# Performance work log

Hardware: AMD Instinct MI355X
Metric: run time of the kernel (lower is better)

Reference implementation:

```python
import jax, jax.numpy as jnp
import numpy as np

H = 12       # num attention heads
D = 64       # head dim
K = 6        # heads activated: max(1, int(H * top_k_percent)), top_k_percent=0.5
EPS = 1e-12  # BERT LayerNorm eps


def setup_inputs() -> dict:
    key = jax.random.key(0)
    ks = jax.random.split(key, 8)
    hid = H * D
    sc = 0.02
    return {
        'hidden_states': jax.random.normal(ks[0], (8, 1024, hid), jnp.float32),
        'Wq': jax.random.normal(ks[1], (hid, hid), jnp.float32) * sc,
        'bq': jnp.zeros((hid,), jnp.float32),
        'Wk': jax.random.normal(ks[2], (hid, hid), jnp.float32) * sc,
        'bk': jnp.zeros((hid,), jnp.float32),
        'Wv': jax.random.normal(ks[3], (hid, hid), jnp.float32) * sc,
        'bv': jnp.zeros((hid,), jnp.float32),
        'Wr': jax.random.normal(ks[4], (hid, H), jnp.float32) * sc,
        'br': jnp.zeros((H,), jnp.float32),
        'Wo': jax.random.normal(ks[5], (hid, hid), jnp.float32) * sc,
        'bo': jnp.zeros((hid,), jnp.float32),
        'ln_g': jnp.ones((hid,), jnp.float32),
        'ln_b': jnp.zeros((hid,), jnp.float32),
    }


def reference(hidden_states, Wq, bq, Wk, bk, Wv, bv, Wr, br, Wo, bo, ln_g, ln_b):
    B, S, hid = hidden_states.shape
    # Router: mean-pooled tokens -> per-head logits -> straight-through top-k mask
    router_in = hidden_states.mean(axis=1)                      # [B, hid]
    logits = router_in @ Wr + br                                # [B, H]
    _, top_idx = jax.lax.top_k(logits, K)                       # [B, K]
    hard = jax.nn.one_hot(top_idx, H, dtype=logits.dtype).sum(axis=1)  # [B, H]
    head_mask = hard + logits - jax.lax.stop_gradient(logits)   # straight-through
    m = head_mask[:, :, None, None]                             # [B, H, 1, 1]

    def proj(W, b):
        return (hidden_states @ W + b).reshape(B, S, H, D).transpose(0, 2, 1, 3)

    q = proj(Wq, bq) * m
    k = proj(Wk, bk) * m
    v = proj(Wv, bv) * m

    scores = jnp.einsum('bhqd,bhkd->bhqk', q, k) / jnp.sqrt(jnp.float32(D))
    probs = jax.nn.softmax(scores, axis=-1)
    ctx = jnp.einsum('bhqk,bhkd->bhqd', probs, v)               # [B, H, S, D]
    ctx = ctx.transpose(0, 2, 1, 3).reshape(B, S, hid)

    # BertSelfOutput: dense -> (dropout=identity in eval) -> residual -> LayerNorm
    x = ctx @ Wo + bo + hidden_states
    mu = x.mean(axis=-1, keepdims=True)
    var = ((x - mu) ** 2).mean(axis=-1, keepdims=True)
    return ((x - mu) / jnp.sqrt(var + EPS)) * ln_g + ln_b
```

## Files before the change

### kernel.cpp

```cpp
#include <hip/hip_runtime.h>

typedef __bf16 bf16;
typedef __bf16 bf16x4_t __attribute__((ext_vector_type(4)));
typedef __bf16 bf16x8 __attribute__((ext_vector_type(8)));
typedef float  f32x4  __attribute__((ext_vector_type(4)));

__device__ __forceinline__ void async16(const void* g, void* l) {
  __builtin_amdgcn_global_load_lds(
      (__attribute__((address_space(1))) void*)(g),
      (__attribute__((address_space(3))) void*)(l), 16, 0, 0);
}

__device__ __forceinline__ f32x4 mfma16(bf16x8 a, bf16x8 b, f32x4 c) {
  return __builtin_amdgcn_mfma_f32_16x16x32_bf16(a, b, c, 0, 0, 0);
}

__global__ __launch_bounds__(256) void cvt_hs_k(const float* __restrict__ src,
                                                bf16* __restrict__ dst, int n) {
  int i = (blockIdx.x * 256 + threadIdx.x) * 4;
  if (i + 3 < n) {
    float4 v = *(const float4*)(src + i);
    dst[i]     = (bf16)v.x;
    dst[i + 1] = (bf16)v.y;
    dst[i + 2] = (bf16)v.z;
    dst[i + 3] = (bf16)v.w;
  } else {
    for (int j = 0; j < 4 && i + j < n; ++j) dst[i + j] = (bf16)src[i + j];
  }
}

__global__ __launch_bounds__(256) void transpose4_k(
    const float* __restrict__ s0, const float* __restrict__ s1,
    const float* __restrict__ s2, const float* __restrict__ s3,
    bf16* __restrict__ d0, bf16* __restrict__ d1,
    bf16* __restrict__ d2, bf16* __restrict__ d3) {
  __shared__ bf16 tile[32][33];
  int z = blockIdx.z;
  const float* in = (z == 0) ? s0 : (z == 1) ? s1 : (z == 2) ? s2 : s3;
  bf16* out       = (z == 0) ? d0 : (z == 1) ? d1 : (z == 2) ? d2 : d3;
  int c0 = blockIdx.x * 32, r0 = blockIdx.y * 32;
  int t = threadIdx.x;
#pragma unroll
  for (int i = 0; i < 4; ++i) {
    int idx = t + i * 256;
    int r = idx >> 5, c = idx & 31;
    tile[r][c] = (bf16)in[(size_t)(r0 + r) * 768 + (c0 + c)];
  }
  __syncthreads();
#pragma unroll
  for (int i = 0; i < 4; ++i) {
    int idx = t + i * 256;
    int r = idx >> 5, c = idx & 31;
    out[(size_t)(c0 + r) * 768 + (r0 + c)] = tile[c][r];
  }
}

__global__ __launch_bounds__(256) void router_partial_k(const float* __restrict__ hs,
                                                        float* __restrict__ partial) {
  int b = blockIdx.x, g = blockIdx.y, t = threadIdx.x;
  if (t >= 192) return;
  const float* p = hs + ((size_t)b * 1024 + g * 64) * 768 + t * 4;
  float4 a = {0.f, 0.f, 0.f, 0.f};
  for (int s = 0; s < 64; ++s) {
    float4 v = *(const float4*)(p + (size_t)s * 768);
    a.x += v.x; a.y += v.y; a.z += v.z; a.w += v.w;
  }
  *(float4*)(partial + ((size_t)b * 16 + g) * 768 + t * 4) = a;
}

__global__ __launch_bounds__(256) void router_final_k(const float* __restrict__ Wr,
                                                      const float* __restrict__ br,
                                                      const float* __restrict__ partial,
                                                      float* __restrict__ mask) {
  int b = blockIdx.x, t = threadIdx.x;
  __shared__ float mean_s[768];
  __shared__ float lg[12];
  for (int c = t; c < 768; c += 256) {
    float a = 0.f;
    for (int g = 0; g < 16; ++g) a += partial[((size_t)b * 16 + g) * 768 + c];
    mean_s[c] = a * (1.0f / 1024.0f);
  }
  __syncthreads();
  if (t < 12) {
    float a = br[t];
    for (int c = 0; c < 768; ++c) a += mean_s[c] * Wr[c * 12 + t];
    lg[t] = a;
  }
  __syncthreads();
  if (t == 0) {
    unsigned chosen = 0;
    for (int j = 0; j < 6; ++j) {
      int bi = -1; float bv = -1e30f;
      for (int h = 0; h < 12; ++h)
        if (!((chosen >> h) & 1) && lg[h] > bv) { bv = lg[h]; bi = h; }
      chosen |= 1u << bi;
    }
    for (int h = 0; h < 12; ++h) mask[b * 12 + h] = ((chosen >> h) & 1) ? 1.f : 0.f;
  }
}

__global__ __launch_bounds__(256, 3) void gemm_qkv_k(
    const bf16* __restrict__ X, const bf16* __restrict__ Wcat,
    const float* __restrict__ bq, const float* __restrict__ bk, const float* __restrict__ bv,
    bf16* __restrict__ Qo, bf16* __restrict__ Ko, bf16* __restrict__ Vto) {
  __shared__ __align__(16) bf16 Al[128 * 64];
  __shared__ __align__(16) bf16 Bl[128 * 64];
  int bid = blockIdx.x;
  int xcd = bid & 7, idx = bid >> 3;
  int nt = idx % 18, mt8 = idx / 18;
  int m0 = (mt8 * 8 + xcd) * 128;
  int n0 = nt * 128;
  int z = nt / 6;
  int nb0 = n0 - z * 768;
  const float* bia = (z == 0) ? bq : (z == 1) ? bk : bv;
  int t = threadIdx.x, w = t >> 6, lane = t & 63, lrow = lane & 15, quad = lane >> 4;
  int wm = (w >> 1) * 64, wn = (w & 1) * 64;

  int srow = t >> 3;
  int sch  = (t & 7) ^ (srow & 7);
  const bf16* aptr[4];
  const bf16* bptr[4];
#pragma unroll
  for (int i = 0; i < 4; ++i) {
    aptr[i] = X    + (size_t)(m0 + i * 32 + srow) * 768 + sch * 8;
    bptr[i] = Wcat + (size_t)(n0 + i * 32 + srow) * 768 + sch * 8;
  }

  int ra_base = wm + lrow, rb_base = wn + lrow;
  const bf16* baA[2];
  const bf16* baB[2];
#pragma unroll
  for (int ks = 0; ks < 2; ++ks) {
    baA[ks] = &Al[ra_base * 64 + (((ks * 4 + quad) ^ (ra_base & 7)) * 8)];
    baB[ks] = &Bl[rb_base * 64 + (((ks * 4 + quad) ^ (rb_base & 7)) * 8)];
  }

  f32x4 acc[4][4];
#pragma unroll
  for (int a = 0; a < 4; ++a)
#pragma unroll
    for (int b = 0; b < 4; ++b) acc[a][b] = (f32x4){0.f, 0.f, 0.f, 0.f};

  for (int k0 = 0; k0 < 768; k0 += 64) {
#pragma unroll
    for (int i = 0; i < 4; ++i) {
      async16(aptr[i], &Al[(i * 256 + t) * 8]);
      aptr[i] += 64;
    }
#pragma unroll
    for (int i = 0; i < 4; ++i) {
      async16(bptr[i], &Bl[(i * 256 + t) * 8]);
      bptr[i] += 64;
    }
    __syncthreads();
    bf16x8 af[2][4], bfr[2][4];
#pragma unroll
    for (int ks = 0; ks < 2; ++ks)
#pragma unroll
      for (int i = 0; i < 4; ++i) {
        af[ks][i]  = *(const bf16x8*)(baA[ks] + i * 1024);
        bfr[ks][i] = *(const bf16x8*)(baB[ks] + i * 1024);
      }
#pragma unroll
    for (int ks = 0; ks < 2; ++ks)
#pragma unroll
      for (int mt = 0; mt < 4; ++mt)
#pragma unroll
        for (int nt2 = 0; nt2 < 4; ++nt2)
          acc[mt][nt2] = mfma16(af[ks][mt], bfr[ks][nt2], acc[mt][nt2]);
    __syncthreads();
  }

  float biasv[4];
#pragma unroll
  for (int nt2 = 0; nt2 < 4; ++nt2) biasv[nt2] = bia[nb0 + wn + nt2 * 16 + lrow];

  if (z == 2) {
#pragma unroll
    for (int mt = 0; mt < 4; ++mt)
#pragma unroll
      for (int nt2 = 0; nt2 < 4; ++nt2) {
        int s_base = m0 + wm + mt * 16 + quad * 4;
        int bb = s_base >> 10, s = s_base & 1023;
        int nl = nb0 + wn + nt2 * 16 + lrow;
        int h = nl >> 6, d = nl & 63;
        bf16x4_t pk;
#pragma unroll
        for (int r = 0; r < 4; ++r) pk[r] = (bf16)(acc[mt][nt2][r] + biasv[nt2]);
        *(bf16x4_t*)&Vto[(((size_t)bb * 12 + h) * 64 + d) * 1024 + s] = pk;
      }
  } else {
    bf16* Out = (z == 0) ? Qo : Ko;
#pragma unroll
    for (int mt = 0; mt < 4; ++mt)
#pragma unroll
      for (int nt2 = 0; nt2 < 4; ++nt2)
#pragma unroll
        for (int r = 0; r < 4; ++r) {
          int m = m0 + wm + mt * 16 + quad * 4 + r;
          int nl = nb0 + wn + nt2 * 16 + lrow;
          int bb = m >> 10, s = m & 1023, h = nl >> 6, d = nl & 63;
          Out[(((size_t)bb * 12 + h) * 1024 + s) * 64 + d] =
              (bf16)(acc[mt][nt2][r] + biasv[nt2]);
        }
  }
}

__global__ __launch_bounds__(256) void attn_k(
    const bf16* __restrict__ Q, const bf16* __restrict__ K, const bf16* __restrict__ Vt,
    const float* __restrict__ mask, bf16* __restrict__ ctx) {
  int qt = blockIdx.x, bh = blockIdx.y;
  int b = bh / 12, h = bh % 12;
  int t = threadIdx.x, w = t >> 6, lane = t & 63, lrow = lane & 15, quad = lane >> 4;

  if (mask[bh] == 0.f) {
    for (int i = t; i < 4096; i += 256) {
      int r = i >> 5, c = i & 31;
      size_t e = ((size_t)(b * 1024 + qt * 128 + r)) * 768 + h * 64;
      ((unsigned*)ctx)[e / 2 + c] = 0u;
    }
    return;
  }

  __shared__ __align__(16) bf16 K_lds[128 * 64];
  __shared__ __align__(16) bf16 V_lds[64 * 128];
  __shared__ __align__(16) bf16 P_lds[4][32 * 136];

  const bf16* Qh = Q  + (size_t)bh * 65536;
  const bf16* Kh = K  + (size_t)bh * 65536;
  const bf16* Vh = Vt + (size_t)bh * 65536;

  bf16x8 qf[2][2];
#pragma unroll
  for (int mt = 0; mt < 2; ++mt)
#pragma unroll
    for (int ks = 0; ks < 2; ++ks)
      qf[mt][ks] = *(const bf16x8*)&Qh[(size_t)(qt * 128 + w * 32 + mt * 16 + lrow) * 64 + ks * 32 + quad * 8];

  f32x4 o_acc[2][4];
  float m_i[2][4], l_i[2][4];
#pragma unroll
  for (int mt = 0; mt < 2; ++mt) {
#pragma unroll
    for (int dt = 0; dt < 4; ++dt) o_acc[mt][dt] = (f32x4){0.f, 0.f, 0.f, 0.f};
#pragma unroll
    for (int r = 0; r < 4; ++r) { m_i[mt][r] = -INFINITY; l_i[mt][r] = 0.f; }
  }

  for (int kt = 0; kt < 8; ++kt) {
#pragma unroll
    for (int i = 0; i < 4; ++i) {
      int c = i * 256 + t;
      int r = c >> 3, ch = (c & 7) ^ (r & 7);
      async16(Kh + (size_t)kt * 8192 + r * 64 + ch * 8, &K_lds[c * 8]);
    }
#pragma unroll
    for (int i = 0; i < 4; ++i) {
      int c = i * 256 + t;
      int r = c >> 4, ch = (c & 15) ^ (r & 7);
      async16(Vh + (size_t)r * 1024 + kt * 128 + ch * 8, &V_lds[c * 8]);
    }
    __syncthreads();

    f32x4 s_acc[2][8];
#pragma unroll
    for (int mt = 0; mt < 2; ++mt)
#pragma unroll
      for (int nt = 0; nt < 8; ++nt) s_acc[mt][nt] = (f32x4){0.f, 0.f, 0.f, 0.f};
#pragma unroll
    for (int nt = 0; nt < 8; ++nt) {
      int rb = nt * 16 + lrow;
#pragma unroll
      for (int ks = 0; ks < 2; ++ks) {
        bf16x8 kf = *(const bf16x8*)&K_lds[rb * 64 + (((ks * 4 + quad) ^ (rb & 7)) * 8)];
        s_acc[0][nt] = mfma16(qf[0][ks], kf, s_acc[0][nt]);
        s_acc[1][nt] = mfma16(qf[1][ks], kf, s_acc[1][nt]);
      }
    }
#pragma unroll
    for (int mt = 0; mt < 2; ++mt)
#pragma unroll
      for (int nt = 0; nt < 8; ++nt) s_acc[mt][nt] = s_acc[mt][nt] * 0.125f;

#pragma unroll
    for (int mt = 0; mt < 2; ++mt) {
#pragma unroll
      for (int r = 0; r < 4; ++r) {
        float mx = s_acc[mt][0][r];
#pragma unroll
        for (int nt = 1; nt < 8; ++nt) mx = fmaxf(mx, s_acc[mt][nt][r]);
        mx = fmaxf(mx, __shfl_xor(mx, 1));
        mx = fmaxf(mx, __shfl_xor(mx, 2));
        mx = fmaxf(mx, __shfl_xor(mx, 4));
        mx = fmaxf(mx, __shfl_xor(mx, 8));
        float mold = m_i[mt][r];
        float mnew = fmaxf(mold, mx);
        float alpha = __expf(mold - mnew);
        m_i[mt][r] = mnew;
        float rs = 0.f;
#pragma unroll
        for (int nt = 0; nt < 8; ++nt) {
          float pv = __expf(s_acc[mt][nt][r] - mnew);
          rs += pv;
          P_lds[w][(mt * 16 + quad * 4 + r) * 136 + nt * 16 + lrow] = (bf16)pv;
        }
        rs += __shfl_xor(rs, 1);
        rs += __shfl_xor(rs, 2);
        rs += __shfl_xor(rs, 4);
        rs += __shfl_xor(rs, 8);
        l_i[mt][r] = l_i[mt][r] * alpha + rs;
#pragma unroll
        for (int dt = 0; dt < 4; ++dt) o_acc[mt][dt][r] *= alpha;
      }
    }
    __syncthreads();

#pragma unroll
    for (int dt = 0; dt < 4; ++dt) {
      int rv = dt * 16 + lrow;
#pragma unroll
      for (int ks = 0; ks < 4; ++ks) {
        bf16x8 vf = *(const bf16x8*)&V_lds[rv * 128 + (((ks * 4 + quad) ^ (rv & 7)) * 8)];
#pragma unroll
        for (int mt = 0; mt < 2; ++mt) {
          bf16x8 pf = *(const bf16x8*)&P_lds[w][(mt * 16 + lrow) * 136 + ks * 32 + quad * 8];
          o_acc[mt][dt] = mfma16(pf, vf, o_acc[mt][dt]);
        }
      }
    }
    __syncthreads();
  }

#pragma unroll
  for (int mt = 0; mt < 2; ++mt)
#pragma unroll
    for (int r = 0; r < 4; ++r) {
      float inv = 1.0f / l_i[mt][r];
      int s = qt * 128 + w * 32 + mt * 16 + quad * 4 + r;
#pragma unroll
      for (int dt = 0; dt < 4; ++dt) {
        int d = dt * 16 + lrow;
        ctx[((size_t)(b * 1024 + s)) * 768 + h * 64 + d] = (bf16)(o_acc[mt][dt][r] * inv);
      }
    }
}

__global__ __launch_bounds__(256, 3) void gemm_out_k(
    const bf16* __restrict__ Cx, const bf16* __restrict__ Wot,
    const float* __restrict__ bo, const float* __restrict__ res,
    float* __restrict__ xo) {
  __shared__ __align__(16) bf16 Al[128 * 64];
  __shared__ __align__(16) bf16 Bl[128 * 64];
  int bid = blockIdx.x;
  int xcd = bid & 7, idx = bid >> 3;
  int nt = idx % 6, mt8 = idx / 6;
  int m0 = (mt8 * 8 + xcd) * 128;
  int n0 = nt * 128;
  int t = threadIdx.x, w = t >> 6, lane = t & 63, lrow = lane & 15, quad = lane >> 4;
  int wm = (w >> 1) * 64, wn = (w & 1) * 64;

  int srow = t >> 3;
  int sch  = (t & 7) ^ (srow & 7);
  const bf16* aptr[4];
  const bf16* bptr[4];
#pragma unroll
  for (int i = 0; i < 4; ++i) {
    aptr[i] = Cx  + (size_t)(m0 + i * 32 + srow) * 768 + sch * 8;
    bptr[i] = Wot + (size_t)(n0 + i * 32 + srow) * 768 + sch * 8;
  }
  int ra_base = wm + lrow, rb_base = wn + lrow;
  const bf16* baA[2];
  const bf16* baB[2];
#pragma unroll
  for (int ks = 0; ks < 2; ++ks) {
    baA[ks] = &Al[ra_base * 64 + (((ks * 4 + quad) ^ (ra_base & 7)) * 8)];
    baB[ks] = &Bl[rb_base * 64 + (((ks * 4 + quad) ^ (rb_base & 7)) * 8)];
  }

  f32x4 acc[4][4];
#pragma unroll
  for (int a = 0; a < 4; ++a)
#pragma unroll
    for (int b = 0; b < 4; ++b) acc[a][b] = (f32x4){0.f, 0.f, 0.f, 0.f};

  for (int k0 = 0; k0 < 768; k0 += 64) {
#pragma unroll
    for (int i = 0; i < 4; ++i) {
      async16(aptr[i], &Al[(i * 256 + t) * 8]);
      aptr[i] += 64;
    }
#pragma unroll
    for (int i = 0; i < 4; ++i) {
      async16(bptr[i], &Bl[(i * 256 + t) * 8]);
      bptr[i] += 64;
    }
    __syncthreads();
    bf16x8 af[2][4], bfr[2][4];
#pragma unroll
    for (int ks = 0; ks < 2; ++ks)
#pragma unroll
      for (int i = 0; i < 4; ++i) {
        af[ks][i]  = *(const bf16x8*)(baA[ks] + i * 1024);
        bfr[ks][i] = *(const bf16x8*)(baB[ks] + i * 1024);
      }
#pragma unroll
    for (int ks = 0; ks < 2; ++ks)
#pragma unroll
      for (int mt = 0; mt < 4; ++mt)
#pragma unroll
        for (int nt2 = 0; nt2 < 4; ++nt2)
          acc[mt][nt2] = mfma16(af[ks][mt], bfr[ks][nt2], acc[mt][nt2]);
    __syncthreads();
  }

  float biasv[4];
#pragma unroll
  for (int nt2 = 0; nt2 < 4; ++nt2) biasv[nt2] = bo[n0 + wn + nt2 * 16 + lrow];

#pragma unroll
  for (int mt = 0; mt < 4; ++mt)
#pragma unroll
    for (int nt2 = 0; nt2 < 4; ++nt2)
#pragma unroll
      for (int r = 0; r < 4; ++r) {
        int m = m0 + wm + mt * 16 + quad * 4 + r;
        int n = n0 + wn + nt2 * 16 + lrow;
        xo[(size_t)m * 768 + n] = acc[mt][nt2][r] + biasv[nt2] + res[(size_t)m * 768 + n];
      }
}

__global__ __launch_bounds__(256) void ln_k(const float* __restrict__ x,
                                            const float* __restrict__ g,
                                            const float* __restrict__ be,
                                            float* __restrict__ out) {
  int row = blockIdx.x, t = threadIdx.x;
  const float* xr = x + (size_t)row * 768;
  float v0 = xr[t], v1 = xr[t + 256], v2 = xr[t + 512];
  float s = v0 + v1 + v2;
  float s2 = v0 * v0 + v1 * v1 + v2 * v2;
#pragma unroll
  for (int off = 32; off > 0; off >>= 1) {
    s  += __shfl_down(s, off);
    s2 += __shfl_down(s2, off);
  }
  __shared__ float red[8];
  if ((t & 63) == 0) { red[(t >> 6) * 2] = s; red[(t >> 6) * 2 + 1] = s2; }
  __syncthreads();
  if (t == 0) {
    float a = 0.f, b2 = 0.f;
    for (int i = 0; i < 4; ++i) { a += red[2 * i]; b2 += red[2 * i + 1]; }
    float mu = a * (1.0f / 768.0f);
    float var = b2 * (1.0f / 768.0f) - mu * mu;
    red[0] = mu;
    red[1] = rsqrtf(var + 1e-12f);
  }
  __syncthreads();
  float mu = red[0], rs = red[1];
  out[(size_t)row * 768 + t]       = (v0 - mu) * rs * g[t]       + be[t];
  out[(size_t)row * 768 + t + 256] = (v1 - mu) * rs * g[t + 256] + be[t + 256];
  out[(size_t)row * 768 + t + 512] = (v2 - mu) * rs * g[t + 512] + be[t + 512];
}

extern "C" void kernel_launch(void* const* d_in, const int* in_sizes, int n_in,
                              void* d_out, int out_size, void* d_ws, size_t ws_size,
                              hipStream_t stream) {
  const float* hs  = (const float*)d_in[0];
  const float* Wq  = (const float*)d_in[1];
  const float* bq  = (const float*)d_in[2];
  const float* Wk  = (const float*)d_in[3];
  const float* bk  = (const float*)d_in[4];
  const float* Wv  = (const float*)d_in[5];
  const float* bv  = (const float*)d_in[6];
  const float* Wr  = (const float*)d_in[7];
  const float* br  = (const float*)d_in[8];
  const float* Wo  = (const float*)d_in[9];
  const float* bo  = (const float*)d_in[10];
  const float* lng = (const float*)d_in[11];
  const float* lnb = (const float*)d_in[12];
  float* out = (float*)d_out;
  dim3 blk(256);

  char* p = (char*)d_ws;
  float* maskp   = (float*)p; p += 512;
  float* partial = (float*)p; p += (size_t)8 * 16 * 768 * 4;
  bf16* hsb  = (bf16*)p; p += (size_t)8192 * 768 * 2;
  bf16* Wcat = (bf16*)p; p += (size_t)2304 * 768 * 2;
  bf16* Wot  = (bf16*)p; p += (size_t)768 * 768 * 2;

  cvt_hs_k<<<dim3(6144), blk, 0, stream>>>(hs, hsb, 6291456);
  transpose4_k<<<dim3(24, 24, 4), blk, 0, stream>>>(
      Wq, Wk, Wv, Wo, Wcat, Wcat + 768 * 768, Wcat + 1536 * 768, Wot);
  router_partial_k<<<dim3(8, 16), blk, 0, stream>>>(hs, partial);
  router_final_k<<<dim3(8), blk, 0, stream>>>(Wr, br, partial, maskp);

  size_t used_common = (size_t)(p - (char*)d_ws);
  size_t need_big = used_common + 3 * (size_t)8192 * 768 * 2;

  if (ws_size >= need_big) {
    char* qk_base = p;
    bf16* Qb  = (bf16*)p; p += (size_t)8192 * 768 * 2;
    bf16* Kb  = (bf16*)p; p += (size_t)8192 * 768 * 2;
    bf16* Vtb = (bf16*)p;
    float* Xb = (float*)qk_base;
    bf16* Ctx = (bf16*)d_out;

    gemm_qkv_k<<<dim3(8 * 8 * 18), blk, 0, stream>>>(hsb, Wcat, bq, bk, bv, Qb, Kb, Vtb);
    attn_k<<<dim3(8, 96), blk, 0, stream>>>(Qb, Kb, Vtb, maskp, Ctx);
    gemm_out_k<<<dim3(8 * 8 * 6), blk, 0, stream>>>(Ctx, Wot, bo, hs, Xb);
    ln_k<<<dim3(8192), blk, 0, stream>>>(Xb, lng, lnb, out);
  } else {
    bf16* Qb  = (bf16*)p; p += (size_t)1024 * 768 * 2;
    bf16* Kb  = (bf16*)p; p += (size_t)1024 * 768 * 2;
    bf16* Vtb = (bf16*)p; p += (size_t)1024 * 768 * 2;
    bf16* Ctx = (bf16*)p; p += (size_t)1024 * 768 * 2;
    float* Xb = (float*)p; p += (size_t)1024 * 768 * 4;

    for (int b = 0; b < 8; ++b) {
      const bf16* hsb_b = hsb + (size_t)b * 1024 * 768;
      const float* hs_b = hs + (size_t)b * 1024 * 768;
      float* outb = out + (size_t)b * 1024 * 768;
      gemm_qkv_k<<<dim3(8 * 1 * 18), blk, 0, stream>>>(hsb_b, Wcat, bq, bk, bv, Qb, Kb, Vtb);
      attn_k<<<dim3(8, 12), blk, 0, stream>>>(Qb, Kb, Vtb, maskp + b * 12, Ctx);
      gemm_out_k<<<dim3(8 * 1 * 6), blk, 0, stream>>>(Ctx, Wot, bo, hs_b, Xb);
      ln_k<<<dim3(1024), blk, 0, stream>>>(Xb, lng, lnb, outb);
    }
  }
}
```

Measured before the change: 252.5 us.

## Skip masked-head GEMM tiles and keep attention probabilities in registers

The QKV projection now exits early for output tiles whose two heads are both masked off. The output projection skips K-chunks that belong to inactive heads, since their context rows are zero. The attention kernel computes S transposed, so row max and sum reductions reduce to cross-quad shuffles, and it builds the P operand for the PV MFMA through lane shuffles instead of an LDS round trip. This removes the per-warp P buffer and one barrier per key tile, at the cost of more shuffle instructions and a changed block order.

```diff
diff --git a/kernel.cpp b/kernel.cpp
--- a/kernel.cpp
+++ b/kernel.cpp
@@ -1,6 +1,7 @@
 #include <hip/hip_runtime.h>
 
 typedef __bf16 bf16;
+typedef __bf16 bf16x2_t __attribute__((ext_vector_type(2)));
 typedef __bf16 bf16x4_t __attribute__((ext_vector_type(4)));
 typedef __bf16 bf16x8 __attribute__((ext_vector_type(8)));
 typedef float  f32x4  __attribute__((ext_vector_type(4)));
@@ -102,6 +103,7 @@
 __global__ __launch_bounds__(256, 3) void gemm_qkv_k(
     const bf16* __restrict__ X, const bf16* __restrict__ Wcat,
     const float* __restrict__ bq, const float* __restrict__ bk, const float* __restrict__ bv,
+    const float* __restrict__ mask,
     bf16* __restrict__ Qo, bf16* __restrict__ Ko, bf16* __restrict__ Vto) {
   __shared__ __align__(16) bf16 Al[128 * 64];
   __shared__ __align__(16) bf16 Bl[128 * 64];
@@ -112,6 +114,9 @@
   int n0 = nt * 128;
   int z = nt / 6;
   int nb0 = n0 - z * 768;
+  int bb = m0 >> 10, hh0 = nb0 >> 6;
+  if (mask[bb * 12 + hh0] == 0.f && mask[bb * 12 + hh0 + 1] == 0.f) return;
+
   const float* bia = (z == 0) ? bq : (z == 1) ? bk : bv;
   int t = threadIdx.x, w = t >> 6, lane = t & 63, lrow = lane & 15, quad = lane >> 4;
   int wm = (w >> 1) * 64, wn = (w & 1) * 64;
@@ -181,13 +186,13 @@
 #pragma unroll
       for (int nt2 = 0; nt2 < 4; ++nt2) {
         int s_base = m0 + wm + mt * 16 + quad * 4;
-        int bb = s_base >> 10, s = s_base & 1023;
+        int bb2 = s_base >> 10, s = s_base & 1023;
         int nl = nb0 + wn + nt2 * 16 + lrow;
         int h = nl >> 6, d = nl & 63;
         bf16x4_t pk;
 #pragma unroll
         for (int r = 0; r < 4; ++r) pk[r] = (bf16)(acc[mt][nt2][r] + biasv[nt2]);
-        *(bf16x4_t*)&Vto[(((size_t)bb * 12 + h) * 64 + d) * 1024 + s] = pk;
+        *(bf16x4_t*)&Vto[(((size_t)bb2 * 12 + h) * 64 + d) * 1024 + s] = pk;
       }
   } else {
     bf16* Out = (z == 0) ? Qo : Ko;
@@ -199,17 +204,17 @@
         for (int r = 0; r < 4; ++r) {
           int m = m0 + wm + mt * 16 + quad * 4 + r;
           int nl = nb0 + wn + nt2 * 16 + lrow;
-          int bb = m >> 10, s = m & 1023, h = nl >> 6, d = nl & 63;
-          Out[(((size_t)bb * 12 + h) * 1024 + s) * 64 + d] =
+          int bb2 = m >> 10, s = m & 1023, h = nl >> 6, d = nl & 63;
+          Out[(((size_t)bb2 * 12 + h) * 1024 + s) * 64 + d] =
               (bf16)(acc[mt][nt2][r] + biasv[nt2]);
         }
   }
 }
 
-__global__ __launch_bounds__(256) void attn_k(
+__global__ __launch_bounds__(256, 4) void attn_k(
     const bf16* __restrict__ Q, const bf16* __restrict__ K, const bf16* __restrict__ Vt,
     const float* __restrict__ mask, bf16* __restrict__ ctx) {
-  int qt = blockIdx.x, bh = blockIdx.y;
+  int bh = blockIdx.x, qt = blockIdx.y;
   int b = bh / 12, h = bh % 12;
   int t = threadIdx.x, w = t >> 6, lane = t & 63, lrow = lane & 15, quad = lane >> 4;
 
@@ -224,7 +229,6 @@
 
   __shared__ __align__(16) bf16 K_lds[128 * 64];
   __shared__ __align__(16) bf16 V_lds[64 * 128];
-  __shared__ __align__(16) bf16 P_lds[4][32 * 136];
 
   const bf16* Qh = Q  + (size_t)bh * 65536;
   const bf16* Kh = K  + (size_t)bh * 65536;
@@ -238,13 +242,13 @@
       qf[mt][ks] = *(const bf16x8*)&Qh[(size_t)(qt * 128 + w * 32 + mt * 16 + lrow) * 64 + ks * 32 + quad * 8];
 
   f32x4 o_acc[2][4];
-  float m_i[2][4], l_i[2][4];
+  float m_i[2], l_i[2];
 #pragma unroll
   for (int mt = 0; mt < 2; ++mt) {
 #pragma unroll
     for (int dt = 0; dt < 4; ++dt) o_acc[mt][dt] = (f32x4){0.f, 0.f, 0.f, 0.f};
-#pragma unroll
-    for (int r = 0; r < 4; ++r) { m_i[mt][r] = -INFINITY; l_i[mt][r] = 0.f; }
+    m_i[mt] = -INFINITY;
+    l_i[mt] = 0.f;
   }
 
   for (int kt = 0; kt < 8; ++kt) {
@@ -262,80 +266,89 @@
     }
     __syncthreads();
 
-    f32x4 s_acc[2][8];
-#pragma unroll
-    for (int mt = 0; mt < 2; ++mt)
-#pragma unroll
-      for (int nt = 0; nt < 8; ++nt) s_acc[mt][nt] = (f32x4){0.f, 0.f, 0.f, 0.f};
-#pragma unroll
-    for (int nt = 0; nt < 8; ++nt) {
-      int rb = nt * 16 + lrow;
-#pragma unroll
-      for (int ks = 0; ks < 2; ++ks) {
-        bf16x8 kf = *(const bf16x8*)&K_lds[rb * 64 + (((ks * 4 + quad) ^ (rb & 7)) * 8)];
-        s_acc[0][nt] = mfma16(qf[0][ks], kf, s_acc[0][nt]);
-        s_acc[1][nt] = mfma16(qf[1][ks], kf, s_acc[1][nt]);
-      }
-    }
-#pragma unroll
-    for (int mt = 0; mt < 2; ++mt)
-#pragma unroll
-      for (int nt = 0; nt < 8; ++nt) s_acc[mt][nt] = s_acc[mt][nt] * 0.125f;
-
 #pragma unroll
     for (int mt = 0; mt < 2; ++mt) {
-#pragma unroll
-      for (int r = 0; r < 4; ++r) {
-        float mx = s_acc[mt][0][r];
-#pragma unroll
-        for (int nt = 1; nt < 8; ++nt) mx = fmaxf(mx, s_acc[mt][nt][r]);
-        mx = fmaxf(mx, __shfl_xor(mx, 1));
-        mx = fmaxf(mx, __shfl_xor(mx, 2));
-        mx = fmaxf(mx, __shfl_xor(mx, 4));
-        mx = fmaxf(mx, __shfl_xor(mx, 8));
-        float mold = m_i[mt][r];
-        float mnew = fmaxf(mold, mx);
-        float alpha = __expf(mold - mnew);
-        m_i[mt][r] = mnew;
-        float rs = 0.f;
-#pragma unroll
-        for (int nt = 0; nt < 8; ++nt) {
-          float pv = __expf(s_acc[mt][nt][r] - mnew);
-          rs += pv;
-          P_lds[w][(mt * 16 + quad * 4 + r) * 136 + nt * 16 + lrow] = (bf16)pv;
+      f32x4 s[8];
+#pragma unroll
+      for (int nt = 0; nt < 8; ++nt) s[nt] = (f32x4){0.f, 0.f, 0.f, 0.f};
+#pragma unroll
+      for (int nt = 0; nt < 8; ++nt) {
+        int rb = nt * 16 + lrow;
+#pragma unroll
+        for (int ks = 0; ks < 2; ++ks) {
+          bf16x8 kf = *(const bf16x8*)&K_lds[rb * 64 + (((ks * 4 + quad) ^ (rb & 7)) * 8)];
+          s[nt] = mfma16(kf, qf[mt][ks], s[nt]);
         }
-        rs += __shfl_xor(rs, 1);
-        rs += __shfl_xor(rs, 2);
-        rs += __shfl_xor(rs, 4);
-        rs += __shfl_xor(rs, 8);
-        l_i[mt][r] = l_i[mt][r] * alpha + rs;
-#pragma unroll
-        for (int dt = 0; dt < 4; ++dt) o_acc[mt][dt][r] *= alpha;
+      }
+      float mx = -INFINITY;
+#pragma unroll
+      for (int nt = 0; nt < 8; ++nt) {
+        s[nt] = s[nt] * 0.125f;
+#pragma unroll
+        for (int r = 0; r < 4; ++r) mx = fmaxf(mx, s[nt][r]);
+      }
+      mx = fmaxf(mx, __shfl_xor(mx, 16));
+      mx = fmaxf(mx, __shfl_xor(mx, 32));
+      float mold = m_i[mt];
+      float mnew = fmaxf(mold, mx);
+      float alpha = __expf(mold - mnew);
+      m_i[mt] = mnew;
+      float rs = 0.f;
+      int pk[8][2];
+#pragma unroll
+      for (int nt = 0; nt < 8; ++nt) {
+        float p0 = __expf(s[nt][0] - mnew);
+        float p1 = __expf(s[nt][1] - mnew);
+        float p2 = __expf(s[nt][2] - mnew);
+        float p3 = __expf(s[nt][3] - mnew);
+        rs += p0 + p1 + p2 + p3;
+        union { bf16x2_t h; int i; } u0, u1;
+        u0.h[0] = (bf16)p0; u0.h[1] = (bf16)p1;
+        u1.h[0] = (bf16)p2; u1.h[1] = (bf16)p3;
+        pk[nt][0] = u0.i;
+        pk[nt][1] = u1.i;
+      }
+      rs += __shfl_xor(rs, 16);
+      rs += __shfl_xor(rs, 32);
+      l_i[mt] = l_i[mt] * alpha + rs;
+      float ar[4];
+#pragma unroll
+      for (int r = 0; r < 4; ++r) ar[r] = __shfl(alpha, quad * 4 + r);
+#pragma unroll
+      for (int dt = 0; dt < 4; ++dt)
+#pragma unroll
+        for (int r = 0; r < 4; ++r) o_acc[mt][dt][r] *= ar[r];
+#pragma unroll
+      for (int ks2 = 0; ks2 < 4; ++ks2) {
+        int pw[4];
+#pragma unroll
+        for (int sI = 0; sI < 4; ++sI) {
+          int src = (((quad & 1) * 2 + (sI >> 1)) << 4) | lrow;
+          int va = __shfl(pk[2 * ks2][sI & 1], src);
+          int vb = __shfl(pk[2 * ks2 + 1][sI & 1], src);
+          pw[sI] = (quad >> 1) ? vb : va;
+        }
+        union { int i[4]; bf16x8 v; } pu;
+        pu.i[0] = pw[0]; pu.i[1] = pw[1]; pu.i[2] = pw[2]; pu.i[3] = pw[3];
+#pragma unroll
+        for (int dt = 0; dt < 4; ++dt) {
+          int rv = dt * 16 + lrow;
+          bf16x8 vf = *(const bf16x8*)&V_lds[rv * 128 + (((ks2 * 4 + quad) ^ (rv & 7)) * 8)];
+          o_acc[mt][dt] = mfma16(pu.v, vf, o_acc[mt][dt]);
+        }
       }
     }
     __syncthreads();
-
-#pragma unroll
-    for (int dt = 0; dt < 4; ++dt) {
-      int rv = dt * 16 + lrow;
-#pragma unroll
-      for (int ks = 0; ks < 4; ++ks) {
-        bf16x8 vf = *(const bf16x8*)&V_lds[rv * 128 + (((ks * 4 + quad) ^ (rv & 7)) * 8)];
-#pragma unroll
-        for (int mt = 0; mt < 2; ++mt) {
-          bf16x8 pf = *(const bf16x8*)&P_lds[w][(mt * 16 + lrow) * 136 + ks * 32 + quad * 8];
-          o_acc[mt][dt] = mfma16(pf, vf, o_acc[mt][dt]);
-        }
-      }
-    }
-    __syncthreads();
-  }
-
-#pragma unroll
-  for (int mt = 0; mt < 2; ++mt)
+  }
+
+#pragma unroll
+  for (int mt = 0; mt < 2; ++mt) {
+    float lr[4];
+#pragma unroll
+    for (int r = 0; r < 4; ++r) lr[r] = __shfl(l_i[mt], quad * 4 + r);
 #pragma unroll
     for (int r = 0; r < 4; ++r) {
-      float inv = 1.0f / l_i[mt][r];
+      float inv = 1.0f / lr[r];
       int s = qt * 128 + w * 32 + mt * 16 + quad * 4 + r;
 #pragma unroll
       for (int dt = 0; dt < 4; ++dt) {
@@ -343,11 +356,13 @@
         ctx[((size_t)(b * 1024 + s)) * 768 + h * 64 + d] = (bf16)(o_acc[mt][dt][r] * inv);
       }
     }
+  }
 }
 
 __global__ __launch_bounds__(256, 3) void gemm_out_k(
     const bf16* __restrict__ Cx, const bf16* __restrict__ Wot,
     const float* __restrict__ bo, const float* __restrict__ res,
+    const float* __restrict__ mask,
     float* __restrict__ xo) {
   __shared__ __align__(16) bf16 Al[128 * 64];
   __shared__ __align__(16) bf16 Bl[128 * 64];
@@ -359,6 +374,12 @@
   int t = threadIdx.x, w = t >> 6, lane = t & 63, lrow = lane & 15, quad = lane >> 4;
   int wm = (w >> 1) * 64, wn = (w & 1) * 64;
 
+  int bb = m0 >> 10;
+  unsigned am = 0;
+#pragma unroll
+  for (int hh = 0; hh < 12; ++hh)
+    am |= (mask[bb * 12 + hh] != 0.f) ? (1u << hh) : 0u;
+
   int srow = t >> 3;
   int sch  = (t & 7) ^ (srow & 7);
   const bf16* aptr[4];
@@ -384,33 +405,31 @@
     for (int b = 0; b < 4; ++b) acc[a][b] = (f32x4){0.f, 0.f, 0.f, 0.f};
 
   for (int k0 = 0; k0 < 768; k0 += 64) {
-#pragma unroll
-    for (int i = 0; i < 4; ++i) {
-      async16(aptr[i], &Al[(i * 256 + t) * 8]);
-      aptr[i] += 64;
-    }
-#pragma unroll
-    for (int i = 0; i < 4; ++i) {
-      async16(bptr[i], &Bl[(i * 256 + t) * 8]);
-      bptr[i] += 64;
-    }
-    __syncthreads();
-    bf16x8 af[2][4], bfr[2][4];
-#pragma unroll
-    for (int ks = 0; ks < 2; ++ks)
-#pragma unroll
-      for (int i = 0; i < 4; ++i) {
-        af[ks][i]  = *(const bf16x8*)(baA[ks] + i * 1024);
-        bfr[ks][i] = *(const bf16x8*)(baB[ks] + i * 1024);
-      }
-#pragma unroll
-    for (int ks = 0; ks < 2; ++ks)
-#pragma unroll
-      for (int mt = 0; mt < 4; ++mt)
-#pragma unroll
-        for (int nt2 = 0; nt2 < 4; ++nt2)
-          acc[mt][nt2] = mfma16(af[ks][mt], bfr[ks][nt2], acc[mt][nt2]);
-    __syncthreads();
+    if (am & (1u << (k0 >> 6))) {
+#pragma unroll
+      for (int i = 0; i < 4; ++i) async16(aptr[i], &Al[(i * 256 + t) * 8]);
+#pragma unroll
+      for (int i = 0; i < 4; ++i) async16(bptr[i], &Bl[(i * 256 + t) * 8]);
+      __syncthreads();
+      bf16x8 af[2][4], bfr[2][4];
+#pragma unroll
+      for (int ks = 0; ks < 2; ++ks)
+#pragma unroll
+        for (int i = 0; i < 4; ++i) {
+          af[ks][i]  = *(const bf16x8*)(baA[ks] + i * 1024);
+          bfr[ks][i] = *(const bf16x8*)(baB[ks] + i * 1024);
+        }
+#pragma unroll
+      for (int ks = 0; ks < 2; ++ks)
+#pragma unroll
+        for (int mt = 0; mt < 4; ++mt)
+#pragma unroll
+          for (int nt2 = 0; nt2 < 4; ++nt2)
+            acc[mt][nt2] = mfma16(af[ks][mt], bfr[ks][nt2], acc[mt][nt2]);
+      __syncthreads();
+    }
+#pragma unroll
+    for (int i = 0; i < 4; ++i) { aptr[i] += 64; bptr[i] += 64; }
   }
 
   float biasv[4];
@@ -504,9 +523,9 @@
     float* Xb = (float*)qk_base;
     bf16* Ctx = (bf16*)d_out;
 
-    gemm_qkv_k<<<dim3(8 * 8 * 18), blk, 0, stream>>>(hsb, Wcat, bq, bk, bv, Qb, Kb, Vtb);
-    attn_k<<<dim3(8, 96), blk, 0, stream>>>(Qb, Kb, Vtb, maskp, Ctx);
-    gemm_out_k<<<dim3(8 * 8 * 6), blk, 0, stream>>>(Ctx, Wot, bo, hs, Xb);
+    gemm_qkv_k<<<dim3(8 * 8 * 18), blk, 0, stream>>>(hsb, Wcat, bq, bk, bv, maskp, Qb, Kb, Vtb);
+    attn_k<<<dim3(96, 8), blk, 0, stream>>>(Qb, Kb, Vtb, maskp, Ctx);
+    gemm_out_k<<<dim3(8 * 8 * 6), blk, 0, stream>>>(Ctx, Wot, bo, hs, maskp, Xb);
     ln_k<<<dim3(8192), blk, 0, stream>>>(Xb, lng, lnb, out);
   } else {
     bf16* Qb  = (bf16*)p; p += (size_t)1024 * 768 * 2;
@@ -519,9 +538,9 @@
       const bf16* hsb_b = hsb + (size_t)b * 1024 * 768;
       const float* hs_b = hs + (size_t)b * 1024 * 768;
       float* outb = out + (size_t)b * 1024 * 768;
-      gemm_qkv_k<<<dim3(8 * 1 * 18), blk, 0, stream>>>(hsb_b, Wcat, bq, bk, bv, Qb, Kb, Vtb);
-      attn_k<<<dim3(8, 12), blk, 0, stream>>>(Qb, Kb, Vtb, maskp + b * 12, Ctx);
-      gemm_out_k<<<dim3(8 * 1 * 6), blk, 0, stream>>>(Ctx, Wot, bo, hs_b, Xb);
+      gemm_qkv_k<<<dim3(8 * 1 * 18), blk, 0, stream>>>(hsb_b, Wcat, bq, bk, bv, maskp + b * 12, Qb, Kb, Vtb);
+      attn_k<<<dim3(12, 8), blk, 0, stream>>>(Qb, Kb, Vtb, maskp + b * 12, Ctx);
+      gemm_out_k<<<dim3(8 * 1 * 6), blk, 0, stream>>>(Ctx, Wot, bo, hs_b, maskp + b * 12, Xb);
       ln_k<<<dim3(1024), blk, 0, stream>>>(Xb, lng, lnb, outb);
     }
   }
```

After: 314.8 us. 24.7% more time.

## Skip masked-head work in QKV and output GEMMs, restructure attention per row-tile

Applied to the files above, without the earlier changes.

The QKV GEMM now exits early for 128-column tiles whose two heads are both masked off by the router, and the output GEMM skips K-chunks that belong to masked heads, since their context is zero. The attention kernel handles one 16-row tile at a time, which halves the P scratch in LDS and drops a barrier; it also swaps grid dimensions so heads vary fastest and sets launch bounds for 3 blocks per CU. About half the heads are masked, so roughly half of the projection and output-GEMM work can be skipped. The skipped Q/K/V buffers are left unwritten, which is safe only because attention already zero-fills masked heads without reading them.

```diff
diff --git a/kernel.cpp b/kernel.cpp
--- a/kernel.cpp
+++ b/kernel.cpp
@@ -1,6 +1,7 @@
 #include <hip/hip_runtime.h>
 
 typedef __bf16 bf16;
+typedef __bf16 bf16x2_t __attribute__((ext_vector_type(2)));
 typedef __bf16 bf16x4_t __attribute__((ext_vector_type(4)));
 typedef __bf16 bf16x8 __attribute__((ext_vector_type(8)));
 typedef float  f32x4  __attribute__((ext_vector_type(4)));
@@ -102,6 +103,7 @@
 __global__ __launch_bounds__(256, 3) void gemm_qkv_k(
     const bf16* __restrict__ X, const bf16* __restrict__ Wcat,
     const float* __restrict__ bq, const float* __restrict__ bk, const float* __restrict__ bv,
+    const float* __restrict__ mask,
     bf16* __restrict__ Qo, bf16* __restrict__ Ko, bf16* __restrict__ Vto) {
   __shared__ __align__(16) bf16 Al[128 * 64];
   __shared__ __align__(16) bf16 Bl[128 * 64];
@@ -112,6 +114,9 @@
   int n0 = nt * 128;
   int z = nt / 6;
   int nb0 = n0 - z * 768;
+  int bb = m0 >> 10, hh0 = nb0 >> 6;
+  if (mask[bb * 12 + hh0] == 0.f && mask[bb * 12 + hh0 + 1] == 0.f) return;
+
   const float* bia = (z == 0) ? bq : (z == 1) ? bk : bv;
   int t = threadIdx.x, w = t >> 6, lane = t & 63, lrow = lane & 15, quad = lane >> 4;
   int wm = (w >> 1) * 64, wn = (w & 1) * 64;
@@ -181,13 +186,13 @@
 #pragma unroll
       for (int nt2 = 0; nt2 < 4; ++nt2) {
         int s_base = m0 + wm + mt * 16 + quad * 4;
-        int bb = s_base >> 10, s = s_base & 1023;
+        int bb2 = s_base >> 10, s = s_base & 1023;
         int nl = nb0 + wn + nt2 * 16 + lrow;
         int h = nl >> 6, d = nl & 63;
         bf16x4_t pk;
 #pragma unroll
         for (int r = 0; r < 4; ++r) pk[r] = (bf16)(acc[mt][nt2][r] + biasv[nt2]);
-        *(bf16x4_t*)&Vto[(((size_t)bb * 12 + h) * 64 + d) * 1024 + s] = pk;
+        *(bf16x4_t*)&Vto[(((size_t)bb2 * 12 + h) * 64 + d) * 1024 + s] = pk;
       }
   } else {
     bf16* Out = (z == 0) ? Qo : Ko;
@@ -199,17 +204,17 @@
         for (int r = 0; r < 4; ++r) {
           int m = m0 + wm + mt * 16 + quad * 4 + r;
           int nl = nb0 + wn + nt2 * 16 + lrow;
-          int bb = m >> 10, s = m & 1023, h = nl >> 6, d = nl & 63;
-          Out[(((size_t)bb * 12 + h) * 1024 + s) * 64 + d] =
+          int bb2 = m >> 10, s = m & 1023, h = nl >> 6, d = nl & 63;
+          Out[(((size_t)bb2 * 12 + h) * 1024 + s) * 64 + d] =
               (bf16)(acc[mt][nt2][r] + biasv[nt2]);
         }
   }
 }
 
-__global__ __launch_bounds__(256) void attn_k(
+__global__ __launch_bounds__(256, 3) void attn_k(
     const bf16* __restrict__ Q, const bf16* __restrict__ K, const bf16* __restrict__ Vt,
     const float* __restrict__ mask, bf16* __restrict__ ctx) {
-  int qt = blockIdx.x, bh = blockIdx.y;
+  int bh = blockIdx.x, qt = blockIdx.y;
   int b = bh / 12, h = bh % 12;
   int t = threadIdx.x, w = t >> 6, lane = t & 63, lrow = lane & 15, quad = lane >> 4;
 
@@ -224,7 +229,7 @@
 
   __shared__ __align__(16) bf16 K_lds[128 * 64];
   __shared__ __align__(16) bf16 V_lds[64 * 128];
-  __shared__ __align__(16) bf16 P_lds[4][32 * 136];
+  __shared__ __align__(16) bf16 P_lds[4][16 * 136];
 
   const bf16* Qh = Q  + (size_t)bh * 65536;
   const bf16* Kh = K  + (size_t)bh * 65536;
@@ -262,33 +267,28 @@
     }
     __syncthreads();
 
-    f32x4 s_acc[2][8];
-#pragma unroll
-    for (int mt = 0; mt < 2; ++mt)
-#pragma unroll
-      for (int nt = 0; nt < 8; ++nt) s_acc[mt][nt] = (f32x4){0.f, 0.f, 0.f, 0.f};
-#pragma unroll
-    for (int nt = 0; nt < 8; ++nt) {
-      int rb = nt * 16 + lrow;
-#pragma unroll
-      for (int ks = 0; ks < 2; ++ks) {
-        bf16x8 kf = *(const bf16x8*)&K_lds[rb * 64 + (((ks * 4 + quad) ^ (rb & 7)) * 8)];
-        s_acc[0][nt] = mfma16(qf[0][ks], kf, s_acc[0][nt]);
-        s_acc[1][nt] = mfma16(qf[1][ks], kf, s_acc[1][nt]);
-      }
-    }
-#pragma unroll
-    for (int mt = 0; mt < 2; ++mt)
-#pragma unroll
-      for (int nt = 0; nt < 8; ++nt) s_acc[mt][nt] = s_acc[mt][nt] * 0.125f;
-
 #pragma unroll
     for (int mt = 0; mt < 2; ++mt) {
+      f32x4 s_acc[8];
+#pragma unroll
+      for (int nt = 0; nt < 8; ++nt) s_acc[nt] = (f32x4){0.f, 0.f, 0.f, 0.f};
+#pragma unroll
+      for (int nt = 0; nt < 8; ++nt) {
+        int rb = nt * 16 + lrow;
+#pragma unroll
+        for (int ks = 0; ks < 2; ++ks) {
+          bf16x8 kf = *(const bf16x8*)&K_lds[rb * 64 + (((ks * 4 + quad) ^ (rb & 7)) * 8)];
+          s_acc[nt] = mfma16(qf[mt][ks], kf, s_acc[nt]);
+        }
+      }
+#pragma unroll
+      for (int nt = 0; nt < 8; ++nt) s_acc[nt] = s_acc[nt] * 0.125f;
+
 #pragma unroll
       for (int r = 0; r < 4; ++r) {
-        float mx = s_acc[mt][0][r];
-#pragma unroll
-        for (int nt = 1; nt < 8; ++nt) mx = fmaxf(mx, s_acc[mt][nt][r]);
+        float mx = s_acc[0][r];
+#pragma unroll
+        for (int nt = 1; nt < 8; ++nt) mx = fmaxf(mx, s_acc[nt][r]);
         mx = fmaxf(mx, __shfl_xor(mx, 1));
         mx = fmaxf(mx, __shfl_xor(mx, 2));
         mx = fmaxf(mx, __shfl_xor(mx, 4));
@@ -300,9 +300,9 @@
         float rs = 0.f;
 #pragma unroll
         for (int nt = 0; nt < 8; ++nt) {
-          float pv = __expf(s_acc[mt][nt][r] - mnew);
+          float pv = __expf(s_acc[nt][r] - mnew);
           rs += pv;
-          P_lds[w][(mt * 16 + quad * 4 + r) * 136 + nt * 16 + lrow] = (bf16)pv;
+          P_lds[w][(quad * 4 + r) * 136 + nt * 16 + lrow] = (bf16)pv;
         }
         rs += __shfl_xor(rs, 1);
         rs += __shfl_xor(rs, 2);
@@ -312,19 +312,18 @@
 #pragma unroll
         for (int dt = 0; dt < 4; ++dt) o_acc[mt][dt][r] *= alpha;
       }
-    }
-    __syncthreads();
-
-#pragma unroll
-    for (int dt = 0; dt < 4; ++dt) {
-      int rv = dt * 16 + lrow;
-#pragma unroll
-      for (int ks = 0; ks < 4; ++ks) {
-        bf16x8 vf = *(const bf16x8*)&V_lds[rv * 128 + (((ks * 4 + quad) ^ (rv & 7)) * 8)];
-#pragma unroll
-        for (int mt = 0; mt < 2; ++mt) {
-          bf16x8 pf = *(const bf16x8*)&P_lds[w][(mt * 16 + lrow) * 136 + ks * 32 + quad * 8];
-          o_acc[mt][dt] = mfma16(pf, vf, o_acc[mt][dt]);
+
+      bf16x8 pf[4];
+#pragma unroll
+      for (int ks = 0; ks < 4; ++ks)
+        pf[ks] = *(const bf16x8*)&P_lds[w][lrow * 136 + ks * 32 + quad * 8];
+#pragma unroll
+      for (int dt = 0; dt < 4; ++dt) {
+        int rv = dt * 16 + lrow;
+#pragma unroll
+        for (int ks = 0; ks < 4; ++ks) {
+          bf16x8 vf = *(const bf16x8*)&V_lds[rv * 128 + (((ks * 4 + quad) ^ (rv & 7)) * 8)];
+          o_acc[mt][dt] = mfma16(pf[ks], vf, o_acc[mt][dt]);
         }
       }
     }
@@ -348,6 +347,7 @@
 __global__ __launch_bounds__(256, 3) void gemm_out_k(
     const bf16* __restrict__ Cx, const bf16* __restrict__ Wot,
     const float* __restrict__ bo, const float* __restrict__ res,
+    const float* __restrict__ mask,
     float* __restrict__ xo) {
   __shared__ __align__(16) bf16 Al[128 * 64];
   __shared__ __align__(16) bf16 Bl[128 * 64];
@@ -359,6 +359,12 @@
   int t = threadIdx.x, w = t >> 6, lane = t & 63, lrow = lane & 15, quad = lane >> 4;
   int wm = (w >> 1) * 64, wn = (w & 1) * 64;
 
+  int bb = m0 >> 10;
+  unsigned am = 0;
+#pragma unroll
+  for (int hh = 0; hh < 12; ++hh)
+    am |= (mask[bb * 12 + hh] != 0.f) ? (1u << hh) : 0u;
+
   int srow = t >> 3;
   int sch  = (t & 7) ^ (srow & 7);
   const bf16* aptr[4];
@@ -384,33 +390,31 @@
     for (int b = 0; b < 4; ++b) acc[a][b] = (f32x4){0.f, 0.f, 0.f, 0.f};
 
   for (int k0 = 0; k0 < 768; k0 += 64) {
-#pragma unroll
-    for (int i = 0; i < 4; ++i) {
-      async16(aptr[i], &Al[(i * 256 + t) * 8]);
-      aptr[i] += 64;
-    }
-#pragma unroll
-    for (int i = 0; i < 4; ++i) {
-      async16(bptr[i], &Bl[(i * 256 + t) * 8]);
-      bptr[i] += 64;
-    }
-    __syncthreads();
-    bf16x8 af[2][4], bfr[2][4];
-#pragma unroll
-    for (int ks = 0; ks < 2; ++ks)
-#pragma unroll
-      for (int i = 0; i < 4; ++i) {
-        af[ks][i]  = *(const bf16x8*)(baA[ks] + i * 1024);
-        bfr[ks][i] = *(const bf16x8*)(baB[ks] + i * 1024);
-      }
-#pragma unroll
-    for (int ks = 0; ks < 2; ++ks)
-#pragma unroll
-      for (int mt = 0; mt < 4; ++mt)
-#pragma unroll
-        for (int nt2 = 0; nt2 < 4; ++nt2)
-          acc[mt][nt2] = mfma16(af[ks][mt], bfr[ks][nt2], acc[mt][nt2]);
-    __syncthreads();
+    if (am & (1u << (k0 >> 6))) {
+#pragma unroll
+      for (int i = 0; i < 4; ++i) async16(aptr[i], &Al[(i * 256 + t) * 8]);
+#pragma unroll
+      for (int i = 0; i < 4; ++i) async16(bptr[i], &Bl[(i * 256 + t) * 8]);
+      __syncthreads();
+      bf16x8 af[2][4], bfr[2][4];
+#pragma unroll
+      for (int ks = 0; ks < 2; ++ks)
+#pragma unroll
+        for (int i = 0; i < 4; ++i) {
+          af[ks][i]  = *(const bf16x8*)(baA[ks] + i * 1024);
+          bfr[ks][i] = *(const bf16x8*)(baB[ks] + i * 1024);
+        }
+#pragma unroll
+      for (int ks = 0; ks < 2; ++ks)
+#pragma unroll
+        for (int mt = 0; mt < 4; ++mt)
+#pragma unroll
+          for (int nt2 = 0; nt2 < 4; ++nt2)
+            acc[mt][nt2] = mfma16(af[ks][mt], bfr[ks][nt2], acc[mt][nt2]);
+      __syncthreads();
+    }
+#pragma unroll
+    for (int i = 0; i < 4; ++i) { aptr[i] += 64; bptr[i] += 64; }
   }
 
   float biasv[4];
@@ -504,9 +508,9 @@
     float* Xb = (float*)qk_base;
     bf16* Ctx = (bf16*)d_out;
 
-    gemm_qkv_k<<<dim3(8 * 8 * 18), blk, 0, stream>>>(hsb, Wcat, bq, bk, bv, Qb, Kb, Vtb);
-    attn_k<<<dim3(8, 96), blk, 0, stream>>>(Qb, Kb, Vtb, maskp, Ctx);
-    gemm_out_k<<<dim3(8 * 8 * 6), blk, 0, stream>>>(Ctx, Wot, bo, hs, Xb);
+    gemm_qkv_k<<<dim3(8 * 8 * 18), blk, 0, stream>>>(hsb, Wcat, bq, bk, bv, maskp, Qb, Kb, Vtb);
+    attn_k<<<dim3(96, 8), blk, 0, stream>>>(Qb, Kb, Vtb, maskp, Ctx);
+    gemm_out_k<<<dim3(8 * 8 * 6), blk, 0, stream>>>(Ctx, Wot, bo, hs, maskp, Xb);
     ln_k<<<dim3(8192), blk, 0, stream>>>(Xb, lng, lnb, out);
   } else {
     bf16* Qb  = (bf16*)p; p += (size_t)1024 * 768 * 2;
@@ -519,9 +523,9 @@
       const bf16* hsb_b = hsb + (size_t)b * 1024 * 768;
       const float* hs_b = hs + (size_t)b * 1024 * 768;
       float* outb = out + (size_t)b * 1024 * 768;
-      gemm_qkv_k<<<dim3(8 * 1 * 18), blk, 0, stream>>>(hsb_b, Wcat, bq, bk, bv, Qb, Kb, Vtb);
-      attn_k<<<dim3(8, 12), blk, 0, stream>>>(Qb, Kb, Vtb, maskp + b * 12, Ctx);
-      gemm_out_k<<<dim3(8 * 1 * 6), blk, 0, stream>>>(Ctx, Wot, bo, hs_b, Xb);
+      gemm_qkv_k<<<dim3(8 * 1 * 18), blk, 0, stream>>>(hsb_b, Wcat, bq, bk, bv, maskp + b * 12, Qb, Kb, Vtb);
+      attn_k<<<dim3(12, 8), blk, 0, stream>>>(Qb, Kb, Vtb, maskp + b * 12, Ctx);
+      gemm_out_k<<<dim3(8 * 1 * 6), blk, 0, stream>>>(Ctx, Wot, bo, hs_b, maskp + b * 12, Xb);
       ln_k<<<dim3(1024), blk, 0, stream>>>(Xb, lng, lnb, outb);
     }
   }
```

Result: no change. 255.7 us (+1.3%).
